# Performance work log

Measured on AMD Instinct MI355X. Metric: run time of the kernel, lower is better.

## Reference

```python
import jax, jax.numpy as jnp
import numpy as np

DT = 0.2
DX = 0.0327249  # 2*pi/192
KPAD = 2  # (kernel_size-1)//2 for 5x5 periodic 'same' padding
# total derivative order of fd00, fd01, fd10, fd02, fd11, fd20
_ORD = np.array([0, 1, 1, 2, 2, 2], dtype=np.float32)
_SCALES = (DX ** -_ORD)  # FD2d scale = dx^-(jx+jy)


def _poly_apply(w0, b0, w1, b1, wf, bf, x):
    # SymNet (expr.poly): each hidden layer computes two linear combos and
    # appends their product as a new channel; final linear -> scalar.
    o = x @ w0.T + b0                                        # [..., 2]
    x = jnp.concatenate([x, o[..., :1] * o[..., 1:2]], -1)   # [..., 13]
    o = x @ w1.T + b1
    x = jnp.concatenate([x, o[..., :1] * o[..., 1:2]], -1)   # [..., 14]
    return (x @ wf.T + bf)[..., 0]


def _rhs(u, kernels, pw0, pb0, pw1, pb1, pwf, pbf):
    # u: [B, C, H, W]
    B, C, H, W = u.shape
    ks = kernels * jnp.asarray(_SCALES, u.dtype)[:, None, None]   # [6,5,5]
    k01f = -ks[1, :, ::-1]   # -flip along width  (torch flip([3]))
    k10f = -ks[2, ::-1, :]   # -flip along height (torch flip([2]))
    kall = jnp.concatenate([ks, k01f[None], k10f[None]], 0)[:, None]  # [8,1,5,5]
    up = jnp.pad(u, ((0, 0), (0, 0), (KPAD, KPAD), (KPAD, KPAD)), mode='wrap')
    up = up.reshape(B * C, 1, H + 2 * KPAD, W + 2 * KPAD)
    D = jax.lax.conv_general_dilated(up, kall, (1, 1), 'VALID')   # [B*C,8,H,W]
    D = D.reshape(B, C, 8, H, W)
    # per-channel blocks ordered (00,01,10,02,11,20)
    base = jnp.transpose(D[:, :, :6], (0, 3, 4, 1, 2)).reshape(B, H, W, C * 6)
    f01 = jnp.transpose(D[:, :, 6], (0, 2, 3, 1))   # [B,H,W,C]
    f10 = jnp.transpose(D[:, :, 7], (0, 2, 3, 1))
    # upwind: pick normal vs flipped 1st-order stencil by sign of d(poly_k)/d(u01/u10)
    Xsel = base
    for k in range(C):
        pk = (pw0[k], pb0[k], pw1[k], pb1[k], pwf[k], pbf[k])
        G = jax.grad(lambda z: _poly_apply(*pk, z).sum())(base)   # [B,H,W,C*6]
        g01, g10 = G[..., k * 6 + 1], G[..., k * 6 + 2]
        u01 = jnp.where(g01 > 0, base[..., k * 6 + 1], f01[..., k])
        u10 = jnp.where(g10 > 0, base[..., k * 6 + 2], f10[..., k])
        Xsel = Xsel.at[..., k * 6 + 1].set(u01).at[..., k * 6 + 2].set(u10)
    uadd = jnp.stack(
        [_poly_apply(pw0[k], pb0[k], pw1[k], pb1[k], pwf[k], pbf[k], Xsel)
         for k in range(C)], axis=1)                              # [B,C,H,W]
    return uadd


def setup_inputs() -> dict:
    key = jax.random.key(0)
    ks = jax.random.split(key, 8)
    f32 = jnp.float32
    inp = {
        'init': jax.random.normal(ks[0], (16, 2, 192, 192), f32),
        'kernels': jax.random.normal(ks[1], (6, 5, 5), f32) * 0.002,
        'poly_w0': jax.random.normal(ks[2], (2, 2, 12), f32) * 0.01,
        'poly_b0': jax.random.normal(ks[3], (2, 2), f32) * 0.01,
        'poly_w1': jax.random.normal(ks[4], (2, 2, 13), f32) * 0.01,
        'poly_b1': jax.random.normal(ks[5], (2, 2), f32) * 0.01,
        'poly_wf': jax.random.normal(ks[6], (2, 1, 14), f32) * 0.01,
        'poly_bf': jax.random.normal(ks[7], (2, 1), f32) * 0.01,
        'T': 1,
    }
    return inp


def reference(init, kernels, poly_w0, poly_b0, poly_w1, poly_b1, poly_wf, poly_bf, T):
    stepnum = int(round(T / DT))  # 5 RK2 (midpoint) steps
    u = init
    for _ in range(stepnum):
        uh = u + (DT / 2) * _rhs(u, kernels, poly_w0, poly_b0, poly_w1, poly_b1, poly_wf, poly_bf)
        u = u + DT * _rhs(uh, kernels, poly_w0, poly_b0, poly_w1, poly_b1, poly_wf, poly_bf)
    return u
```

## Files before the change

### kernel.cpp

```cpp
#include <hip/hip_runtime.h>

typedef float v2f __attribute__((ext_vector_type(2)));

#define HH 192
#define WW 192
#define BATCH 16
#define PLANE (HH*WW)
#define NELEM (BATCH*2*PLANE)

#define TILEX 96
#define TILEY 8
#define SW 100
#define SH2 12
#define NPAIR 600

__global__ void prep_kernel(const float* __restrict__ kern,
                            const float* __restrict__ pw0, const float* __restrict__ pb0,
                            const float* __restrict__ pw1, const float* __restrict__ pb1,
                            const float* __restrict__ pwf, const float* __restrict__ pbf,
                            float* __restrict__ ws)
{
    int t = blockIdx.x * blockDim.x + threadIdx.x;
    if (t < 200) {
        const float inv  = 1.0f / 0.0327249f;
        const float inv2 = inv * inv;
        const float sc[6] = {1.0f, inv, inv, inv2, inv2, inv2};
        int o = t / 8, j = t % 8, dy = o / 5, dx = o % 5;
        float v;
        if (j < 6)       v =  kern[j*25 + dy*5 + dx] * sc[j];
        else if (j == 6) v = -kern[1*25 + dy*5 + (4-dx)] * sc[1];
        else             v = -kern[2*25 + (4-dy)*5 + dx] * sc[2];
        ws[o*8 + j] = v;
    } else if (t < 279) {
        int p = t - 200;
        int arr, a, b;
        if (p < 12)       { arr=0; a=p;      b=24+p; }
        else if (p < 24)  { int i=p-12; arr=0; a=12+i; b=36+i; }
        else if (p == 24) { arr=1; a=0; b=2; }
        else if (p == 25) { arr=1; a=1; b=3; }
        else if (p < 38)  { int i=p-26; arr=2; a=i;    b=26+i; }
        else if (p < 50)  { int i=p-38; arr=2; a=13+i; b=39+i; }
        else if (p == 50) { arr=2; a=12; b=38; }
        else if (p == 51) { arr=2; a=25; b=51; }
        else if (p == 52) { arr=3; a=0; b=2; }
        else if (p == 53) { arr=3; a=1; b=3; }
        else if (p < 68)  { int i=p-54; arr=4; a=i; b=14+i; }
        else if (p == 68) { arr=5; a=0; b=1; }
        else {
            const signed char   A0[10] = {1,2,13,14,1,2,14,15,1,2};
            const signed char   A1[10] = {31,32,43,44,33,34,46,47,21,22};
            const unsigned char AR[10] = {0,0,0,0,2,2,2,2,4,4};
            int i = p - 69; arr = AR[i]; a = A0[i]; b = A1[i];
        }
        const float* bases[6] = {pw0, pb0, pw1, pb1, pwf, pbf};
        v2f v; v[0] = bases[arr][a]; v[1] = bases[arr][b];
        ((v2f*)(ws + 256))[p] = v;
    }
}

__global__ __launch_bounds__(256, 3) void rhs_kernel(
    const float* __restrict__ uin,
    const float* __restrict__ ubase,
    float* __restrict__ uout,
    const float* __restrict__ ws,
    float alpha)
{
    const float* K8T = ws;
    const v2f* PP = (const v2f*)(ws + 256);

    __shared__ v2f sh[SH2][SW];
    const int b   = blockIdx.z;
    const int ty0 = blockIdx.y * TILEY;
    const int tx0 = blockIdx.x * TILEX;
    const int tid = threadIdx.x;
    const size_t bo = (size_t)b * 2 * PLANE;

    const float* uin_b = uin + bo;
    for (int i = tid; i < NPAIR; i += 256) {
        const int ly  = i / 50;
        const int cp  = i - ly * 50;
        const int col = cp * 2;
        int gy = ty0 + ly - 2;  if (gy < 0) gy += HH; else if (gy >= HH) gy -= HH;
        int gx0 = tx0 + col - 2; if (gx0 < 0) gx0 += WW; else if (gx0 >= WW) gx0 -= WW;
        const int gi = gy*WW + gx0;
        const float2 a = *(const float2*)(uin_b + gi);
        const float2 c = *(const float2*)(uin_b + PLANE + gi);
        float4 st; st.x = a.x; st.y = c.x; st.z = a.y; st.w = c.y;
        *(float4*)&sh[ly][col] = st;
    }
    __syncthreads();

    const int cy = tid >> 5;
    const int x3 = (tid & 31) * 3;

    v2f D2[3][8];
    #pragma unroll
    for (int p = 0; p < 3; ++p)
        #pragma unroll
        for (int j = 0; j < 8; ++j)
            D2[p][j] = (v2f){0.0f, 0.0f};

    #pragma unroll 1
    for (int dy = 0; dy < 5; ++dy) {
        v2f row[7];
        #pragma unroll
        for (int dx = 0; dx < 7; ++dx)
            row[dx] = sh[cy + dy][x3 + dx];
        const float* Kt = K8T + dy * 40;
        #pragma unroll
        for (int dx = 0; dx < 5; ++dx) {
            #pragma unroll
            for (int j = 0; j < 8; ++j) {
                const float w = Kt[dx*8 + j];
                D2[0][j] += row[dx]   * w;
                D2[1][j] += row[dx+1] * w;
                D2[2][j] += row[dx+2] * w;
            }
        }
    }

#define Z(p,i) (D2[p][(i)%6][(i)/6])

    v2f res[3];
    #pragma unroll
    for (int p = 0; p < 3; ++p) {
        v2f o0 = PP[24], o1 = PP[25];
        #pragma unroll
        for (int i = 0; i < 12; ++i) {
            const float zv = Z(p, i);
            o0 += PP[i]    * zv;
            o1 += PP[12+i] * zv;
        }
        const v2f pb = o0 * o1;
        v2f q0 = PP[52] + PP[50]*pb;
        v2f q1 = PP[53] + PP[51]*pb;
        v2f yb = PP[68] + PP[66]*pb;
        #pragma unroll
        for (int i = 0; i < 12; ++i) {
            const float zv = Z(p, i);
            q0 += PP[26+i] * zv;
            q1 += PP[38+i] * zv;
            yb += PP[54+i] * zv;
        }

        const v2f t1 = o1*PP[69] + o0*PP[71];
        const v2f g1 = PP[77] + PP[66]*t1
            + PP[67]*(q1*(PP[73] + PP[50]*t1) + q0*(PP[75] + PP[51]*t1));
        const v2f t2 = o1*PP[70] + o0*PP[72];
        const v2f g2 = PP[78] + PP[66]*t2
            + PP[67]*(q1*(PP[74] + PP[50]*t2) + q0*(PP[76] + PP[51]*t2));

        const float d1 = (g1[0] > 0.0f) ? 0.0f : (D2[p][6][0] - Z(p,1));
        const float d2 = (g2[0] > 0.0f) ? 0.0f : (D2[p][7][0] - Z(p,2));
        const float d3 = (g1[1] > 0.0f) ? 0.0f : (D2[p][6][1] - Z(p,7));
        const float d4 = (g2[1] > 0.0f) ? 0.0f : (D2[p][7][1] - Z(p,8));

        v2f f0 = o0 + PP[1]*d1;  f0 += PP[2]*d2;  f0 += PP[7]*d3;  f0 += PP[8]*d4;
        v2f f1 = o1 + PP[13]*d1; f1 += PP[14]*d2; f1 += PP[19]*d3; f1 += PP[20]*d4;
        const v2f pf = f0 * f1;
        const v2f dp = pf - pb;
        v2f r0 = q0 + PP[27]*d1; r0 += PP[28]*d2; r0 += PP[33]*d3; r0 += PP[34]*d4;
        r0 += PP[50]*dp;
        v2f r1 = q1 + PP[39]*d1; r1 += PP[40]*d2; r1 += PP[45]*d3; r1 += PP[46]*d4;
        r1 += PP[51]*dp;
        v2f y  = yb + PP[55]*d1; y  += PP[56]*d2; y  += PP[61]*d3; y  += PP[62]*d4;
        y  += PP[66]*dp;
        res[p] = y + PP[67]*(r0*r1);
    }

    const int oy = ty0 + cy, ox = tx0 + x3;
    const size_t o0i = bo + (size_t)oy * WW + ox;
    float bb0[3], bb1[3];
    if (ubase == uin) {
        #pragma unroll
        for (int p = 0; p < 3; ++p) {
            const v2f c = sh[cy+2][x3+2+p];
            bb0[p] = c[0]; bb1[p] = c[1];
        }
    } else {
        #pragma unroll
        for (int p = 0; p < 3; ++p) {
            bb0[p] = ubase[o0i + p];
            bb1[p] = ubase[o0i + PLANE + p];
        }
    }
    #pragma unroll
    for (int p = 0; p < 3; ++p) {
        uout[o0i + p]         = bb0[p] + alpha * res[p][0];
        uout[o0i + PLANE + p] = bb1[p] + alpha * res[p][1];
    }
}

extern "C" void kernel_launch(void* const* d_in, const int* in_sizes, int n_in,
                              void* d_out, int out_size, void* d_ws, size_t ws_size,
                              hipStream_t stream)
{
    const float* init = (const float*)d_in[0];
    const float* kern = (const float*)d_in[1];
    const float* pw0  = (const float*)d_in[2];
    const float* pb0  = (const float*)d_in[3];
    const float* pw1  = (const float*)d_in[4];
    const float* pb1  = (const float*)d_in[5];
    const float* pwf  = (const float*)d_in[6];
    const float* pbf  = (const float*)d_in[7];
    float* out = (float*)d_out;
    float* ws  = (float*)d_ws;

    float* bufA = ws + 512;
    float* bufH = bufA + NELEM;

    prep_kernel<<<dim3(1), dim3(320), 0, stream>>>(kern, pw0, pb0, pw1, pb1, pwf, pbf, ws);

    const dim3 grid(WW/TILEX, HH/TILEY, BATCH);
    const dim3 block(256);
    const float DTF = 0.2f, DTH = 0.1f;

    rhs_kernel<<<grid, block, 0, stream>>>(init, init, bufH, ws, DTH);
    rhs_kernel<<<grid, block, 0, stream>>>(bufH, init, bufA, ws, DTF);
    for (int s = 0; s < 3; ++s) {
        rhs_kernel<<<grid, block, 0, stream>>>(bufA, bufA, bufH, ws, DTH);
        rhs_kernel<<<grid, block, 0, stream>>>(bufH, bufA, bufA, ws, DTF);
    }
    rhs_kernel<<<grid, block, 0, stream>>>(bufA, bufA, bufH, ws, DTH);
    rhs_kernel<<<grid, block, 0, stream>>>(bufH, bufA, out,  ws, DTF);
}
```

Measured before the change: 198.1 us.

## Store intermediate RK states channel-interleaved and prefetch base values before barrier

```diff
diff --git a/kernel.cpp b/kernel.cpp
--- a/kernel.cpp
+++ b/kernel.cpp
@@ -13,6 +13,11 @@
 #define SW 100
 #define SH2 12
 #define NPAIR 600
+
+#define M_INP  1
+#define M_BLDS 2
+#define M_BPLN 4
+#define M_OUTP 8
 
 __global__ void prep_kernel(const float* __restrict__ kern,
                             const float* __restrict__ pw0, const float* __restrict__ pb0,
@@ -63,7 +68,7 @@
     const float* __restrict__ ubase,
     float* __restrict__ uout,
     const float* __restrict__ ws,
-    float alpha)
+    float alpha, int mode)
 {
     const float* K8T = ws;
     const v2f* PP = (const v2f*)(ws + 256);
@@ -75,23 +80,63 @@
     const int tid = threadIdx.x;
     const size_t bo = (size_t)b * 2 * PLANE;
 
-    const float* uin_b = uin + bo;
-    for (int i = tid; i < NPAIR; i += 256) {
-        const int ly  = i / 50;
-        const int cp  = i - ly * 50;
-        const int col = cp * 2;
-        int gy = ty0 + ly - 2;  if (gy < 0) gy += HH; else if (gy >= HH) gy -= HH;
-        int gx0 = tx0 + col - 2; if (gx0 < 0) gx0 += WW; else if (gx0 >= WW) gx0 -= WW;
-        const int gi = gy*WW + gx0;
-        const float2 a = *(const float2*)(uin_b + gi);
-        const float2 c = *(const float2*)(uin_b + PLANE + gi);
-        float4 st; st.x = a.x; st.y = c.x; st.z = a.y; st.w = c.y;
-        *(float4*)&sh[ly][col] = st;
-    }
-    __syncthreads();
+    if (mode & M_INP) {
+        const float* uin_b = uin + bo;
+        for (int i = tid; i < NPAIR; i += 256) {
+            const int ly  = i / 50;
+            const int cp  = i - ly * 50;
+            const int col = cp * 2;
+            int gy = ty0 + ly - 2;  if (gy < 0) gy += HH; else if (gy >= HH) gy -= HH;
+            int gx0 = tx0 + col - 2; if (gx0 < 0) gx0 += WW; else if (gx0 >= WW) gx0 -= WW;
+            const int gi = gy*WW + gx0;
+            const float2 a = *(const float2*)(uin_b + gi);
+            const float2 c = *(const float2*)(uin_b + PLANE + gi);
+            float4 st; st.x = a.x; st.y = c.x; st.z = a.y; st.w = c.y;
+            *(float4*)&sh[ly][col] = st;
+        }
+    } else {
+        const v2f* uin_i = (const v2f*)uin + (size_t)b * PLANE;
+        for (int i = tid; i < NPAIR; i += 256) {
+            const int ly  = i / 50;
+            const int cp  = i - ly * 50;
+            const int col = cp * 2;
+            int gy = ty0 + ly - 2;  if (gy < 0) gy += HH; else if (gy >= HH) gy -= HH;
+            int gx0 = tx0 + col - 2; if (gx0 < 0) gx0 += WW; else if (gx0 >= WW) gx0 -= WW;
+            *(float4*)&sh[ly][col] = *(const float4*)(uin_i + gy*WW + gx0);
+        }
+    }
 
     const int cy = tid >> 5;
     const int x3 = (tid & 31) * 3;
+    const int oy = ty0 + cy, ox = tx0 + x3;
+    const size_t o0i = bo + (size_t)oy * WW + ox;
+    const size_t si  = (size_t)b * PLANE + (size_t)oy * WW + ox;
+
+    float bb0[3], bb1[3];
+    if (!(mode & M_BLDS)) {
+        if (mode & M_BPLN) {
+            #pragma unroll
+            for (int p = 0; p < 3; ++p) {
+                bb0[p] = ubase[o0i + p];
+                bb1[p] = ubase[o0i + PLANE + p];
+            }
+        } else {
+            const v2f* ub = (const v2f*)ubase;
+            #pragma unroll
+            for (int p = 0; p < 3; ++p) {
+                const v2f c = ub[si + p];
+                bb0[p] = c[0]; bb1[p] = c[1];
+            }
+        }
+    }
+    __syncthreads();
+    if (mode & M_BLDS) {
+        #pragma unroll
+        for (int p = 0; p < 3; ++p) {
+            const v2f c = sh[cy+2][x3+2+p];
+            bb0[p] = c[0]; bb1[p] = c[1];
+        }
+    }
 
     v2f D2[3][8];
     #pragma unroll
@@ -168,26 +213,21 @@
         res[p] = y + PP[67]*(r0*r1);
     }
 
-    const int oy = ty0 + cy, ox = tx0 + x3;
-    const size_t o0i = bo + (size_t)oy * WW + ox;
-    float bb0[3], bb1[3];
-    if (ubase == uin) {
+    if (mode & M_OUTP) {
         #pragma unroll
         for (int p = 0; p < 3; ++p) {
-            const v2f c = sh[cy+2][x3+2+p];
-            bb0[p] = c[0]; bb1[p] = c[1];
+            uout[o0i + p]         = bb0[p] + alpha * res[p][0];
+            uout[o0i + PLANE + p] = bb1[p] + alpha * res[p][1];
         }
     } else {
+        v2f* uo = (v2f*)uout;
         #pragma unroll
         for (int p = 0; p < 3; ++p) {
-            bb0[p] = ubase[o0i + p];
-            bb1[p] = ubase[o0i + PLANE + p];
-        }
-    }
-    #pragma unroll
-    for (int p = 0; p < 3; ++p) {
-        uout[o0i + p]         = bb0[p] + alpha * res[p][0];
-        uout[o0i + PLANE + p] = bb1[p] + alpha * res[p][1];
+            v2f w;
+            w[0] = bb0[p] + alpha * res[p][0];
+            w[1] = bb1[p] + alpha * res[p][1];
+            uo[si + p] = w;
+        }
     }
 }
 
@@ -215,12 +255,12 @@
     const dim3 block(256);
     const float DTF = 0.2f, DTH = 0.1f;
 
-    rhs_kernel<<<grid, block, 0, stream>>>(init, init, bufH, ws, DTH);
-    rhs_kernel<<<grid, block, 0, stream>>>(bufH, init, bufA, ws, DTF);
+    rhs_kernel<<<grid, block, 0, stream>>>(init, init, bufH, ws, DTH, M_INP|M_BLDS);
+    rhs_kernel<<<grid, block, 0, stream>>>(bufH, init, bufA, ws, DTF, M_BPLN);
     for (int s = 0; s < 3; ++s) {
-        rhs_kernel<<<grid, block, 0, stream>>>(bufA, bufA, bufH, ws, DTH);
-        rhs_kernel<<<grid, block, 0, stream>>>(bufH, bufA, bufA, ws, DTF);
-    }
-    rhs_kernel<<<grid, block, 0, stream>>>(bufA, bufA, bufH, ws, DTH);
-    rhs_kernel<<<grid, block, 0, stream>>>(bufH, bufA, out,  ws, DTF);
+        rhs_kernel<<<grid, block, 0, stream>>>(bufA, bufA, bufH, ws, DTH, M_BLDS);
+        rhs_kernel<<<grid, block, 0, stream>>>(bufH, bufA, bufA, ws, DTF, 0);
+    }
+    rhs_kernel<<<grid, block, 0, stream>>>(bufA, bufA, bufH, ws, DTH, M_BLDS);
+    rhs_kernel<<<grid, block, 0, stream>>>(bufH, bufA, out,  ws, DTF, M_OUTP);
 }
```

Measured after the change: 189.1 us. -4.5%, faster.
